# Kernel optimization log

Measured on AMD Instinct MI355X. Metric: run time of the kernel, lower is better.

Reference implementation:

```python
import jax, jax.numpy as jnp
import numpy as np

N = 100000   # nodes
E = 3200000  # edges (avg degree 32)
D = 128      # node_input_dim
H = 32       # hidden_dim
OUT = 3


def setup_inputs() -> dict:
    key = jax.random.key(0)
    ks = jax.random.split(key, 8)
    x = jax.random.normal(ks[0], (N, D), jnp.float32)
    edge_index = jax.random.randint(ks[1], (2, E), 0, N, dtype=jnp.int32)
    W1 = jax.random.normal(ks[2], (D, H), jnp.float32) * (1.0 / np.sqrt(D))
    b1 = jnp.zeros((H,), jnp.float32)
    W2 = jax.random.normal(ks[3], (H, H), jnp.float32) * (1.0 / np.sqrt(H))
    b2 = jnp.zeros((H,), jnp.float32)
    Wfc = jax.random.normal(ks[4], (H, OUT), jnp.float32) * (1.0 / np.sqrt(H))
    bfc = jnp.zeros((OUT,), jnp.float32)
    return {"x": x, "edge_index": edge_index, "W1": W1, "b1": b1,
            "W2": W2, "b2": b2, "Wfc": Wfc, "bfc": bfc}


def gcn_conv(x, W, b, src, dst, num_nodes):
    # PyG GCNConv defaults: transform, add self-loops, symmetric deg^-1/2 norm, bias.
    h = x @ W  # [N, H]
    ones = jnp.ones(src.shape[0], x.dtype)
    # degree with self-loop (+1), counted at target index (col) as in PyG
    deg = jax.ops.segment_sum(ones, dst, num_segments=num_nodes) + 1.0
    norm = jax.lax.rsqrt(deg)  # [N]
    coef = norm[src] * norm[dst]  # [E]
    msg = h[src] * coef[:, None]  # [E, H] gather + scale
    agg = jax.ops.segment_sum(msg, dst, num_segments=num_nodes)  # scatter-add
    # self-loop contribution: norm[i]^2 * h[i]
    agg = agg + h * (norm * norm)[:, None]
    return agg + b


def reference(x, edge_index, W1, b1, W2, b2, Wfc, bfc):
    src, dst = edge_index[0], edge_index[1]
    n = x.shape[0]
    h = jax.nn.relu(gcn_conv(x, W1, b1, src, dst, n))
    h = jax.nn.relu(gcn_conv(h, W2, b2, src, dst, n))
    return jax.nn.sigmoid(h @ Wfc + bfc)
```

## Files before the change

kernel.cpp:

```cpp
#include <hip/hip_runtime.h>
#include <hip/hip_fp16.h>
#include <math.h>

#define D_IN   128
#define H_DIM  32
#define OUT_DIM 3

#define BS      256
#define LOGBS   8
#define CAP_B   9088
#define TPB_P   512
#define EPB_P   16384
#define VPT_P   (EPB_P / TPB_P)
#define NB_MAX  1024

static __device__ inline unsigned int h2u(__half2 h) {
    union { __half2 h; unsigned int u; } c; c.h = h; return c.u;
}
static __device__ inline __half2 u2h(unsigned int u) {
    union { unsigned int u; __half2 h; } c; c.u = u; return c.h;
}
static __device__ inline __half2 sh2(__half2 v, int o) {
    return u2h((unsigned int)__shfl_xor((int)h2u(v), o));
}


__global__ __launch_bounds__(TPB_P) void k_part(
    const int* __restrict__ src, const int* __restrict__ dst,
    int* __restrict__ bcur, int* __restrict__ tmcsr, int e, int nb)
{
    __shared__ int hist[NB_MAX];
    __shared__ int cur[NB_MAX];
    const int t = threadIdx.x;
    for (int j = t; j < nb; j += TPB_P) hist[j] = 0;
    __syncthreads();

    const int base = blockIdx.x * EPB_P;
    int d[VPT_P], s[VPT_P];
#pragma unroll
    for (int k = 0; k < VPT_P; ++k) {
        int i = base + k * TPB_P + t;
        if (i < e) {
            d[k] = dst[i];
            s[k] = src[i];
            atomicAdd(&hist[d[k] >> LOGBS], 1);
        } else d[k] = -1;
    }
    __syncthreads();
    for (int j = t; j < nb; j += TPB_P)
        cur[j] = hist[j] ? atomicAdd(&bcur[j], hist[j]) : 0;
    __syncthreads();
#pragma unroll
    for (int k = 0; k < VPT_P; ++k) {
        if (d[k] >= 0) {
            int b = d[k] >> LOGBS;
            int pos = atomicAdd(&cur[b], 1);
            if (pos < CAP_B)
                tmcsr[b * CAP_B + pos] = s[k] | ((d[k] & (BS - 1)) << 17);
        }
    }
}


__global__ __launch_bounds__(512) void k_build(
    int* __restrict__ tmcsr, const int* __restrict__ bcur,
    int* __restrict__ offs, int* __restrict__ ends, float* __restrict__ norm,
    int n)
{
    __shared__ int cnt[BS];
    __shared__ int ss[BS];
    __shared__ int slice[CAP_B];

    const int t = threadIdx.x;
    const int b = blockIdx.x;
    const int bo = b * CAP_B;
    int m = bcur[b];
    if (m > CAP_B) m = CAP_B;

    if (t < BS) cnt[t] = 0;
    __syncthreads();

    for (int i = t; i < m; i += 512)
        atomicAdd(&cnt[tmcsr[bo + i] >> 17], 1);
    __syncthreads();

    int c0 = 0;
    if (t < BS) { c0 = cnt[t]; ss[t] = c0; }
    __syncthreads();
    for (int off = 1; off < BS; off <<= 1) {
        int u = 0;
        if (t < BS && t >= off) u = ss[t - off];
        __syncthreads();
        if (t < BS) ss[t] += u;
        __syncthreads();
    }
    if (t < BS) {
        int eb = ss[t] - c0;
        int node = (b << LOGBS) + t;
        if (node < n) {
            offs[node] = bo + eb;
            ends[node] = bo + eb + c0;
            norm[node] = rsqrtf((float)c0 + 1.0f);
        }
        cnt[t] = eb;
    }
    __syncthreads();

    for (int i = t; i < m; i += 512) {
        int p = tmcsr[bo + i];
        int pos = atomicAdd(&cnt[p >> 17], 1);
        if (pos < CAP_B) slice[pos] = p & 0x1FFFF;
    }
    __syncthreads();

    for (int i = t; i < m; i += 512) tmcsr[bo + i] = slice[i];
}


__global__ __launch_bounds__(512) void k_gemm1(
    const float* __restrict__ x, const float* __restrict__ W1,
    const float* __restrict__ norm, __half* __restrict__ h1s, int n)
{
    __shared__ float Wl[D_IN * H_DIM];
    for (int i = threadIdx.x; i < D_IN * H_DIM; i += 512) Wl[i] = W1[i];
    __syncthreads();

    const int t = threadIdx.x;
    const int jg = t & 3;
    const int node = blockIdx.x * 128 + (t >> 2);
    if (node >= n) return;
    const int j0 = jg * 8;

    float acc[8];
#pragma unroll
    for (int j = 0; j < 8; ++j) acc[j] = 0.0f;

    const float* xrow = &x[(size_t)node * D_IN];
    for (int k = 0; k < D_IN; k += 4) {
        const float4 xv = *(const float4*)&xrow[k];
#pragma unroll
        for (int kk = 0; kk < 4; ++kk) {
            const float xs = (kk == 0) ? xv.x : (kk == 1) ? xv.y
                           : (kk == 2) ? xv.z : xv.w;
            const float4 wa = *(const float4*)&Wl[(k + kk) * H_DIM + j0];
            const float4 wb = *(const float4*)&Wl[(k + kk) * H_DIM + j0 + 4];
            acc[0] = fmaf(xs, wa.x, acc[0]);
            acc[1] = fmaf(xs, wa.y, acc[1]);
            acc[2] = fmaf(xs, wa.z, acc[2]);
            acc[3] = fmaf(xs, wa.w, acc[3]);
            acc[4] = fmaf(xs, wb.x, acc[4]);
            acc[5] = fmaf(xs, wb.y, acc[5]);
            acc[6] = fmaf(xs, wb.z, acc[6]);
            acc[7] = fmaf(xs, wb.w, acc[7]);
        }
    }

    const float nr = norm[node];
    uint4 pk;
    pk.x = h2u(__floats2half2_rn(acc[0]*nr, acc[1]*nr));
    pk.y = h2u(__floats2half2_rn(acc[2]*nr, acc[3]*nr));
    pk.z = h2u(__floats2half2_rn(acc[4]*nr, acc[5]*nr));
    pk.w = h2u(__floats2half2_rn(acc[6]*nr, acc[7]*nr));
    *(uint4*)&h1s[(size_t)node * H_DIM + j0] = pk;
}


__global__ __launch_bounds__(256) void k_gather_g2(
    const __half* __restrict__ hsA, const float* __restrict__ norm,
    const int* __restrict__ offs, const int* __restrict__ ends,
    const int* __restrict__ csr, const float* __restrict__ b1,
    const float* __restrict__ W2, __half* __restrict__ hsB, int n)
{
    __shared__ float Wl[H_DIM * 33];
    __shared__ float bl[H_DIM];
    __shared__ float sout[4][33];
    for (int i = threadIdx.x; i < H_DIM * H_DIM; i += 256) {
        int k = i >> 5, j = i & 31;
        Wl[k * 33 + j] = W2[i];
    }
    if (threadIdx.x < H_DIM) bl[threadIdx.x] = b1[threadIdx.x];
    __syncthreads();

    const int t = threadIdx.x;
    const int w = t >> 6;
    const int node = blockIdx.x * 4 + w;
    if (node >= n) return;
    const int lane = t & 63;
    const int g = lane >> 3;
    const int q = lane & 7;

    const int beg = offs[node];
    const int end = ends[node];
    const uint2* rows = (const uint2*)hsA;

    uint2 rs = rows[node * 8 + q];

    __half2 acc0 = u2h(0u), acc1 = u2h(0u);
    int j = beg + g;
    for (; j + 24 < end; j += 32) {
        int s0 = csr[j];
        int s1 = csr[j + 8];
        int s2 = csr[j + 16];
        int s3 = csr[j + 24];
        uint2 r0 = rows[s0 * 8 + q];
        uint2 r1 = rows[s1 * 8 + q];
        uint2 r2 = rows[s2 * 8 + q];
        uint2 r3 = rows[s3 * 8 + q];
        acc0 = __hadd2(acc0, __hadd2(__hadd2(u2h(r0.x), u2h(r1.x)),
                                     __hadd2(u2h(r2.x), u2h(r3.x))));
        acc1 = __hadd2(acc1, __hadd2(__hadd2(u2h(r0.y), u2h(r1.y)),
                                     __hadd2(u2h(r2.y), u2h(r3.y))));
    }
    for (; j < end; j += 8) {
        uint2 r0 = rows[csr[j] * 8 + q];
        acc0 = __hadd2(acc0, u2h(r0.x));
        acc1 = __hadd2(acc1, u2h(r0.y));
    }
    if (g == 0) {
        acc0 = __hadd2(acc0, u2h(rs.x));
        acc1 = __hadd2(acc1, u2h(rs.y));
    }

#pragma unroll
    for (int o = 8; o < 64; o <<= 1) {
        acc0 = __hadd2(acc0, sh2(acc0, o));
        acc1 = __hadd2(acc1, sh2(acc1, o));
    }

    const float nr = norm[node];
    float2 f0 = __half22float2(acc0);
    float2 f1 = __half22float2(acc1);
    const int kb = q * 4;
    float u0 = fmaxf(fmaf(f0.x, nr, bl[kb + 0]), 0.f);
    float u1 = fmaxf(fmaf(f0.y, nr, bl[kb + 1]), 0.f);
    float u2 = fmaxf(fmaf(f1.x, nr, bl[kb + 2]), 0.f);
    float u3 = fmaxf(fmaf(f1.y, nr, bl[kb + 3]), 0.f);

    float p[4];
#pragma unroll
    for (int jj = 0; jj < 4; ++jj) {
        int jc = g + 8 * jj;
        p[jj] = u0 * Wl[(kb + 0) * 33 + jc]
              + u1 * Wl[(kb + 1) * 33 + jc]
              + u2 * Wl[(kb + 2) * 33 + jc]
              + u3 * Wl[(kb + 3) * 33 + jc];
    }
#pragma unroll
    for (int o = 1; o < 8; o <<= 1) {
        p[0] += __shfl_xor(p[0], o); p[1] += __shfl_xor(p[1], o);
        p[2] += __shfl_xor(p[2], o); p[3] += __shfl_xor(p[3], o);
    }

    if (q == 0) {
        sout[w][g]      = p[0] * nr;
        sout[w][g + 8]  = p[1] * nr;
        sout[w][g + 16] = p[2] * nr;
        sout[w][g + 24] = p[3] * nr;
    }
    if (lane < 8) {
        float4 v = *(float4*)&sout[w][lane * 4];
        uint2 wv;
        wv.x = h2u(__floats2half2_rn(v.x, v.y));
        wv.y = h2u(__floats2half2_rn(v.z, v.w));
        ((uint2*)hsB)[node * 8 + lane] = wv;
    }
}


__global__ __launch_bounds__(256) void k_gather_fin(
    const __half* __restrict__ hs, const float* __restrict__ norm,
    const int* __restrict__ offs, const int* __restrict__ ends,
    const int* __restrict__ csr, const float* __restrict__ b2,
    const float* __restrict__ Wfc, const float* __restrict__ bfc,
    float* __restrict__ out, int n)
{
    const int t = threadIdx.x;
    const int node = blockIdx.x * 4 + (t >> 6);
    if (node >= n) return;
    const int lane = t & 63;
    const int g = lane >> 3;
    const int q = lane & 7;

    const int beg = offs[node];
    const int end = ends[node];
    const uint2* rows = (const uint2*)hs;

    uint2 rs = rows[node * 8 + q];

    __half2 acc0 = u2h(0u), acc1 = u2h(0u);
    int j = beg + g;
    for (; j + 24 < end; j += 32) {
        int s0 = csr[j];
        int s1 = csr[j + 8];
        int s2 = csr[j + 16];
        int s3 = csr[j + 24];
        uint2 r0 = rows[s0 * 8 + q];
        uint2 r1 = rows[s1 * 8 + q];
        uint2 r2 = rows[s2 * 8 + q];
        uint2 r3 = rows[s3 * 8 + q];
        acc0 = __hadd2(acc0, __hadd2(__hadd2(u2h(r0.x), u2h(r1.x)),
                                     __hadd2(u2h(r2.x), u2h(r3.x))));
        acc1 = __hadd2(acc1, __hadd2(__hadd2(u2h(r0.y), u2h(r1.y)),
                                     __hadd2(u2h(r2.y), u2h(r3.y))));
    }
    for (; j < end; j += 8) {
        uint2 r0 = rows[csr[j] * 8 + q];
        acc0 = __hadd2(acc0, u2h(r0.x));
        acc1 = __hadd2(acc1, u2h(r0.y));
    }
    if (g == 0) {
        acc0 = __hadd2(acc0, u2h(rs.x));
        acc1 = __hadd2(acc1, u2h(rs.y));
    }

#pragma unroll
    for (int o = 8; o < 64; o <<= 1) {
        acc0 = __hadd2(acc0, sh2(acc0, o));
        acc1 = __hadd2(acc1, sh2(acc1, o));
    }

    const float nr = norm[node];
    float2 f0 = __half22float2(acc0);
    float2 f1 = __half22float2(acc1);
    const int f = q * 4;
    float v0 = fmaxf(fmaf(f0.x, nr, b2[f + 0]), 0.f);
    float v1 = fmaxf(fmaf(f0.y, nr, b2[f + 1]), 0.f);
    float v2 = fmaxf(fmaf(f1.x, nr, b2[f + 2]), 0.f);
    float v3 = fmaxf(fmaf(f1.y, nr, b2[f + 3]), 0.f);
    float p0 = v0*Wfc[(f+0)*3+0] + v1*Wfc[(f+1)*3+0] + v2*Wfc[(f+2)*3+0] + v3*Wfc[(f+3)*3+0];
    float p1 = v0*Wfc[(f+0)*3+1] + v1*Wfc[(f+1)*3+1] + v2*Wfc[(f+2)*3+1] + v3*Wfc[(f+3)*3+1];
    float p2 = v0*Wfc[(f+0)*3+2] + v1*Wfc[(f+1)*3+2] + v2*Wfc[(f+2)*3+2] + v3*Wfc[(f+3)*3+2];
#pragma unroll
    for (int o = 1; o < 8; o <<= 1) {
        p0 += __shfl_xor(p0, o); p1 += __shfl_xor(p1, o); p2 += __shfl_xor(p2, o);
    }

    if (lane == 0) {
        out[(size_t)node * 3 + 0] = 1.0f / (1.0f + expf(-(p0 + bfc[0])));
        out[(size_t)node * 3 + 1] = 1.0f / (1.0f + expf(-(p1 + bfc[1])));
        out[(size_t)node * 3 + 2] = 1.0f / (1.0f + expf(-(p2 + bfc[2])));
    }
}


extern "C" void kernel_launch(void* const* d_in, const int* in_sizes, int n_in,
                              void* d_out, int out_size, void* d_ws, size_t ws_size,
                              hipStream_t stream)
{
    const float* x   = (const float*)d_in[0];
    const int*   ei  = (const int*)d_in[1];
    const float* W1  = (const float*)d_in[2];
    const float* b1  = (const float*)d_in[3];
    const float* W2  = (const float*)d_in[4];
    const float* b2  = (const float*)d_in[5];
    const float* Wfc = (const float*)d_in[6];
    const float* bfc = (const float*)d_in[7];
    float* out = (float*)d_out;

    const int n = in_sizes[0] / D_IN;
    const int e = in_sizes[1] / 2;
    const int* src = ei;
    const int* dst = ei + e;
    const int nb = (n + BS - 1) >> LOGBS;

    size_t nAl = ((size_t)n + 256) & ~(size_t)255;

    float* norm  = (float*)d_ws;
    int*   offs  = (int*)(norm + nAl);
    int*   ends  = offs + nAl;
    int*   bcur  = ends + nAl;
    int*   tmcsr = bcur + 1024;
    __half* HbA  = (__half*)(tmcsr + (size_t)nb * CAP_B);
    __half* HbB  = HbA + nAl * H_DIM;

    const int nb_gm = (n + 127) / 128;
    const int nb_p  = (e + EPB_P - 1) / EPB_P;
    const int nb_g  = (n + 3) / 4;

    hipMemsetAsync(bcur, 0, (size_t)nb * sizeof(int), stream);
    k_part <<<nb_p, TPB_P, 0, stream>>>(src, dst, bcur, tmcsr, e, nb);
    k_build<<<nb, 512, 0, stream>>>(tmcsr, bcur, offs, ends, norm, n);

    k_gemm1<<<nb_gm, 512, 0, stream>>>(x, W1, norm, HbA, n);

    k_gather_g2<<<nb_g, 256, 0, stream>>>(HbA, norm, offs, ends, tmcsr,
                                          b1, W2, HbB, n);

    k_gather_fin<<<nb_g, 256, 0, stream>>>(HbB, norm, offs, ends, tmcsr,
                                           b2, Wfc, bfc, out, n);
}
```

Baseline: 202.6 us.

## Merge edge partition and first GEMM into one launch, apply norm in build

The edge-partition kernel and the x@W1 GEMM now run as one launch, with block ranges split by blockIdx, so the two independent jobs can overlap on the GPU. Because norm is not known when the GEMM runs, the GEMM writes unscaled fp16 rows and the build kernel rescales each node's row by its norm after computing degrees. This removes one launch and the serial dependency of the GEMM on build, at the cost of an extra read-modify-write of the h1 buffer and a second fp16 rounding.

```diff
diff --git a/kernel.cpp b/kernel.cpp
--- a/kernel.cpp
+++ b/kernel.cpp
@@ -20,44 +20,94 @@
 static __device__ inline __half2 u2h(unsigned int u) {
     union { unsigned int u; __half2 h; } c; c.u = u; return c.h;
 }
+static __device__ inline float2 u2f2(unsigned int u) {
+    union { unsigned int u; __half2 h; } c; c.u = u;
+    return __half22float2(c.h);
+}
 static __device__ inline __half2 sh2(__half2 v, int o) {
     return u2h((unsigned int)__shfl_xor((int)h2u(v), o));
 }
 
 
-__global__ __launch_bounds__(TPB_P) void k_part(
+__global__ __launch_bounds__(TPB_P) void k_front(
     const int* __restrict__ src, const int* __restrict__ dst,
-    int* __restrict__ bcur, int* __restrict__ tmcsr, int e, int nb)
+    int* __restrict__ bcur, int* __restrict__ tmcsr, int e, int nb, int nbp,
+    const float* __restrict__ x, const float* __restrict__ W1,
+    __half* __restrict__ h1u, int n)
 {
-    __shared__ int hist[NB_MAX];
-    __shared__ int cur[NB_MAX];
+    __shared__ float shmem[D_IN * H_DIM];
     const int t = threadIdx.x;
-    for (int j = t; j < nb; j += TPB_P) hist[j] = 0;
-    __syncthreads();
-
-    const int base = blockIdx.x * EPB_P;
-    int d[VPT_P], s[VPT_P];
-#pragma unroll
-    for (int k = 0; k < VPT_P; ++k) {
-        int i = base + k * TPB_P + t;
-        if (i < e) {
-            d[k] = dst[i];
-            s[k] = src[i];
-            atomicAdd(&hist[d[k] >> LOGBS], 1);
-        } else d[k] = -1;
-    }
-    __syncthreads();
-    for (int j = t; j < nb; j += TPB_P)
-        cur[j] = hist[j] ? atomicAdd(&bcur[j], hist[j]) : 0;
-    __syncthreads();
-#pragma unroll
-    for (int k = 0; k < VPT_P; ++k) {
-        if (d[k] >= 0) {
-            int b = d[k] >> LOGBS;
-            int pos = atomicAdd(&cur[b], 1);
-            if (pos < CAP_B)
-                tmcsr[b * CAP_B + pos] = s[k] | ((d[k] & (BS - 1)) << 17);
+
+    if (blockIdx.x < nbp) {
+        int* hist = (int*)shmem;
+        int* cur  = hist + NB_MAX;
+        for (int j = t; j < nb; j += TPB_P) hist[j] = 0;
+        __syncthreads();
+
+        const int base = blockIdx.x * EPB_P;
+        int d[VPT_P], s[VPT_P];
+#pragma unroll
+        for (int k = 0; k < VPT_P; ++k) {
+            int i = base + k * TPB_P + t;
+            if (i < e) {
+                d[k] = dst[i];
+                s[k] = src[i];
+                atomicAdd(&hist[d[k] >> LOGBS], 1);
+            } else d[k] = -1;
         }
+        __syncthreads();
+        for (int j = t; j < nb; j += TPB_P)
+            cur[j] = hist[j] ? atomicAdd(&bcur[j], hist[j]) : 0;
+        __syncthreads();
+#pragma unroll
+        for (int k = 0; k < VPT_P; ++k) {
+            if (d[k] >= 0) {
+                int b = d[k] >> LOGBS;
+                int pos = atomicAdd(&cur[b], 1);
+                if (pos < CAP_B)
+                    tmcsr[b * CAP_B + pos] = s[k] | ((d[k] & (BS - 1)) << 17);
+            }
+        }
+    } else {
+        float* Wl = shmem;
+        for (int i = t; i < D_IN * H_DIM; i += TPB_P) Wl[i] = W1[i];
+        __syncthreads();
+
+        const int jg = t & 3;
+        const int node = (blockIdx.x - nbp) * 128 + (t >> 2);
+        if (node >= n) return;
+        const int j0 = jg * 8;
+
+        float acc[8];
+#pragma unroll
+        for (int j = 0; j < 8; ++j) acc[j] = 0.0f;
+
+        const float* xrow = &x[(size_t)node * D_IN];
+        for (int k = 0; k < D_IN; k += 4) {
+            const float4 xv = *(const float4*)&xrow[k];
+#pragma unroll
+            for (int kk = 0; kk < 4; ++kk) {
+                const float xs = (kk == 0) ? xv.x : (kk == 1) ? xv.y
+                               : (kk == 2) ? xv.z : xv.w;
+                const float4 wa = *(const float4*)&Wl[(k + kk) * H_DIM + j0];
+                const float4 wb = *(const float4*)&Wl[(k + kk) * H_DIM + j0 + 4];
+                acc[0] = fmaf(xs, wa.x, acc[0]);
+                acc[1] = fmaf(xs, wa.y, acc[1]);
+                acc[2] = fmaf(xs, wa.z, acc[2]);
+                acc[3] = fmaf(xs, wa.w, acc[3]);
+                acc[4] = fmaf(xs, wb.x, acc[4]);
+                acc[5] = fmaf(xs, wb.y, acc[5]);
+                acc[6] = fmaf(xs, wb.z, acc[6]);
+                acc[7] = fmaf(xs, wb.w, acc[7]);
+            }
+        }
+
+        uint4 pk;
+        pk.x = h2u(__floats2half2_rn(acc[0], acc[1]));
+        pk.y = h2u(__floats2half2_rn(acc[2], acc[3]));
+        pk.z = h2u(__floats2half2_rn(acc[4], acc[5]));
+        pk.w = h2u(__floats2half2_rn(acc[6], acc[7]));
+        *(uint4*)&h1u[(size_t)node * H_DIM + j0] = pk;
     }
 }
 
@@ -65,7 +115,7 @@
 __global__ __launch_bounds__(512) void k_build(
     int* __restrict__ tmcsr, const int* __restrict__ bcur,
     int* __restrict__ offs, int* __restrict__ ends, float* __restrict__ norm,
-    int n)
+    __half* __restrict__ h1, int n)
 {
     __shared__ int cnt[BS];
     __shared__ int ss[BS];
@@ -94,13 +144,15 @@
         if (t < BS) ss[t] += u;
         __syncthreads();
     }
+    float nrv = 0.f;
+    int node = (b << LOGBS) + (t & (BS - 1));
     if (t < BS) {
         int eb = ss[t] - c0;
-        int node = (b << LOGBS) + t;
+        nrv = rsqrtf((float)c0 + 1.0f);
         if (node < n) {
             offs[node] = bo + eb;
             ends[node] = bo + eb + c0;
-            norm[node] = rsqrtf((float)c0 + 1.0f);
+            norm[node] = nrv;
         }
         cnt[t] = eb;
     }
@@ -114,54 +166,18 @@
     __syncthreads();
 
     for (int i = t; i < m; i += 512) tmcsr[bo + i] = slice[i];
-}
-
-
-__global__ __launch_bounds__(512) void k_gemm1(
-    const float* __restrict__ x, const float* __restrict__ W1,
-    const float* __restrict__ norm, __half* __restrict__ h1s, int n)
-{
-    __shared__ float Wl[D_IN * H_DIM];
-    for (int i = threadIdx.x; i < D_IN * H_DIM; i += 512) Wl[i] = W1[i];
-    __syncthreads();
-
-    const int t = threadIdx.x;
-    const int jg = t & 3;
-    const int node = blockIdx.x * 128 + (t >> 2);
-    if (node >= n) return;
-    const int j0 = jg * 8;
-
-    float acc[8];
-#pragma unroll
-    for (int j = 0; j < 8; ++j) acc[j] = 0.0f;
-
-    const float* xrow = &x[(size_t)node * D_IN];
-    for (int k = 0; k < D_IN; k += 4) {
-        const float4 xv = *(const float4*)&xrow[k];
-#pragma unroll
-        for (int kk = 0; kk < 4; ++kk) {
-            const float xs = (kk == 0) ? xv.x : (kk == 1) ? xv.y
-                           : (kk == 2) ? xv.z : xv.w;
-            const float4 wa = *(const float4*)&Wl[(k + kk) * H_DIM + j0];
-            const float4 wb = *(const float4*)&Wl[(k + kk) * H_DIM + j0 + 4];
-            acc[0] = fmaf(xs, wa.x, acc[0]);
-            acc[1] = fmaf(xs, wa.y, acc[1]);
-            acc[2] = fmaf(xs, wa.z, acc[2]);
-            acc[3] = fmaf(xs, wa.w, acc[3]);
-            acc[4] = fmaf(xs, wb.x, acc[4]);
-            acc[5] = fmaf(xs, wb.y, acc[5]);
-            acc[6] = fmaf(xs, wb.z, acc[6]);
-            acc[7] = fmaf(xs, wb.w, acc[7]);
+
+    if (t < BS && node < n) {
+        uint4* row = (uint4*)&h1[(size_t)node * H_DIM];
+#define SC(v) h2u(__floats2half2_rn(u2f2(v).x * nrv, u2f2(v).y * nrv))
+#pragma unroll
+        for (int r = 0; r < 4; ++r) {
+            uint4 a = row[r];
+            a.x = SC(a.x); a.y = SC(a.y); a.z = SC(a.z); a.w = SC(a.w);
+            row[r] = a;
         }
-    }
-
-    const float nr = norm[node];
-    uint4 pk;
-    pk.x = h2u(__floats2half2_rn(acc[0]*nr, acc[1]*nr));
-    pk.y = h2u(__floats2half2_rn(acc[2]*nr, acc[3]*nr));
-    pk.z = h2u(__floats2half2_rn(acc[4]*nr, acc[5]*nr));
-    pk.w = h2u(__floats2half2_rn(acc[6]*nr, acc[7]*nr));
-    *(uint4*)&h1s[(size_t)node * H_DIM + j0] = pk;
+#undef SC
+    }
 }
 
 
@@ -373,15 +389,15 @@
     __half* HbA  = (__half*)(tmcsr + (size_t)nb * CAP_B);
     __half* HbB  = HbA + nAl * H_DIM;
 
+    const int nb_p  = (e + EPB_P - 1) / EPB_P;
     const int nb_gm = (n + 127) / 128;
-    const int nb_p  = (e + EPB_P - 1) / EPB_P;
     const int nb_g  = (n + 3) / 4;
 
     hipMemsetAsync(bcur, 0, (size_t)nb * sizeof(int), stream);
-    k_part <<<nb_p, TPB_P, 0, stream>>>(src, dst, bcur, tmcsr, e, nb);
-    k_build<<<nb, 512, 0, stream>>>(tmcsr, bcur, offs, ends, norm, n);
-
-    k_gemm1<<<nb_gm, 512, 0, stream>>>(x, W1, norm, HbA, n);
+    k_front<<<nb_p + nb_gm, TPB_P, 0, stream>>>(
+        src, dst, bcur, tmcsr, e, nb, nb_p, x, W1, HbA, n);
+
+    k_build<<<nb, 512, 0, stream>>>(tmcsr, bcur, offs, ends, norm, HbA, n);
 
     k_gather_g2<<<nb_g, 256, 0, stream>>>(HbA, norm, offs, ends, tmcsr,
                                           b1, W2, HbB, n);
```

Result: faster. 188.0 us (-7.2%).
